# Kernel optimization log

Measured on AMD Instinct MI355X. Metric: run time of the kernel, lower is better.

Reference implementation:

```python
import jax, jax.numpy as jnp
import numpy as np

HIDDEN = 300
DEPTH = 6
ATOM_FDIM = 136
BOND_FDIM = 12
BOND_IN = ATOM_FDIM + BOND_FDIM  # 148
MAX_NB = 6
N_MOLS = 4096
ATOMS_PER_MOL = 32
N_ATOMS = N_MOLS * ATOMS_PER_MOL  # 131072
N_BONDS = 2 * N_ATOMS            # 262144 directed bonds


def setup_inputs() -> dict:
    key = jax.random.key(0)
    ks = jax.random.split(key, 11)
    fatoms = jax.random.normal(ks[0], (N_ATOMS, ATOM_FDIM), jnp.float32)
    fbonds = jax.random.normal(ks[1], (N_BONDS, BOND_IN), jnp.float32)
    agraph = jax.random.randint(ks[2], (N_ATOMS, MAX_NB), 0, N_BONDS, jnp.int32)
    bgraph = jax.random.randint(ks[3], (N_BONDS, MAX_NB), 0, N_BONDS, jnp.int32)
    # Linear weights stored pre-transposed so forward is x @ W
    W_i = jax.random.normal(ks[4], (BOND_IN, HIDDEN), jnp.float32) / np.sqrt(BOND_IN)
    W_h = jax.random.normal(ks[5], (HIDDEN, HIDDEN), jnp.float32) / np.sqrt(HIDDEN)
    W_o = jax.random.normal(ks[6], (ATOM_FDIM + HIDDEN, HIDDEN), jnp.float32) / np.sqrt(ATOM_FDIM + HIDDEN)
    b_o = jax.random.normal(ks[7], (HIDDEN,), jnp.float32) * 0.01
    W_a = jax.random.normal(ks[8], (HIDDEN, HIDDEN), jnp.float32) / np.sqrt(HIDDEN)
    W_b = jax.random.normal(ks[9], (HIDDEN, HIDDEN), jnp.float32) / np.sqrt(HIDDEN)
    b_b = jax.random.normal(ks[10], (HIDDEN,), jnp.float32) * 0.01
    return {"fatoms": fatoms, "fbonds": fbonds, "agraph": agraph, "bgraph": bgraph,
            "W_i": W_i, "W_h": W_h, "W_o": W_o, "b_o": b_o,
            "W_a": W_a, "W_b": W_b, "b_b": b_b}


def reference(fatoms, fbonds, agraph, bgraph, W_i, W_h, W_o, b_o, W_a, W_b, b_b):
    # D-MPNN bond message passing (dropout=0.0 -> identity)
    binput = fbonds @ W_i                         # [N_b, H]
    message = jax.nn.relu(binput)
    for _ in range(DEPTH - 1):
        nei = jnp.take(message, bgraph, axis=0).sum(axis=1)   # gather [N_b, MAX_NB, H] -> sum
        message = jax.nn.relu(binput + nei @ W_h)
    nei_a = jnp.take(message, agraph, axis=0).sum(axis=1)     # [N_a, H]
    atom_hiddens = jax.nn.relu(jnp.concatenate([fatoms, nei_a], axis=1) @ W_o + b_o)
    # Per-molecule self-attention pooling (fixed-size scope: ATOMS_PER_MOL atoms/mol)
    h = atom_hiddens.reshape(N_MOLS, ATOMS_PER_MOL, HIDDEN)   # [B, A, H]
    q = jnp.einsum('bah,hk->bak', h, W_a)
    att = jax.nn.softmax(jnp.einsum('bak,bck->bac', q, h), axis=-1)
    att_h = jax.nn.relu(jnp.einsum('bac,bch->bah', att, h) @ W_b + b_b)
    mol_vecs = (h + att_h).sum(axis=1) / ATOMS_PER_MOL        # [B, H]
    return mol_vecs
```

## Files before the change

### kernel.cpp

```cpp
#include <hip/hip_runtime.h>
#include <hip/hip_fp16.h>
#include <math.h>

#define HIDDEN 300
#define ATOM_FDIM 136
#define BOND_IN 148
#define MAX_NB 6
#define N_MOLS 4096
#define APM 32
#define N_ATOMS (N_MOLS*APM)
#define N_BONDS (2*N_ATOMS)

#define BK 16
#define BM 64
#define ASTR 68
#define BSTR 304

#define WT_C 304
#define WT_K 320

typedef unsigned short u16;
typedef short bf16x8 __attribute__((ext_vector_type(8)));
typedef float f32x4  __attribute__((ext_vector_type(4)));

__device__ float g_scratch[3ull * N_BONDS * HIDDEN + (size_t)N_MOLS * HIDDEN + WT_C * WT_K];

__device__ __forceinline__ u16 bf16_rne(float x) {
    unsigned u = __float_as_uint(x);
    unsigned r = (u + 0x7fffu + ((u >> 16) & 1u)) >> 16;
    return (u16)r;
}
__device__ __forceinline__ float bf16_f(u16 h) {
    return __uint_as_float(((unsigned)h) << 16);
}
__device__ __forceinline__ void st_h4(__half* p, float a, float b, float c, float d) {
    *(__half2*)(p)     = __floats2half2_rn(a, b);
    *(__half2*)(p + 2) = __floats2half2_rn(c, d);
}

__global__ __launch_bounds__(256)
void wt_prep(const float* __restrict__ W, u16* __restrict__ wt_hi, u16* __restrict__ wt_lo)
{
    const int i = blockIdx.x * 256 + threadIdx.x;
    if (i >= WT_C * WT_K) return;
    const int c = i / WT_K, k = i - c * WT_K;
    float w = (c < HIDDEN && k < HIDDEN) ? W[(size_t)k * HIDDEN + c] : 0.f;
    const u16 hi = bf16_rne(w);
    const u16 lo = bf16_rne(w - bf16_f(hi));
    wt_hi[i] = hi;
    wt_lo[i] = lo;
}

__global__ __launch_bounds__(512, 4)
void mp_mfma(const __half* __restrict__ msg,
             const int*   __restrict__ graph,
             const u16*   __restrict__ wt_hi,
             const u16*   __restrict__ wt_lo,
             const __half* __restrict__ binput,
             __half* __restrict__ out0)
{
    __shared__ u16 Ahi[64 * 40];
    __shared__ u16 Alo[64 * 40];
    __shared__ int gx[64 * MAX_NB];

    const int tid  = threadIdx.x;
    const int row0 = blockIdx.x * 64;

    if (tid < 64 * MAX_NB) gx[tid] = graph[(size_t)row0 * MAX_NB + tid];
    __syncthreads();

    const int w  = tid >> 6;
    const int l  = tid & 63;
    const int g  = l >> 4;
    const int mr = (w & 3) * 16 + (l & 15);
    const int tbase = (w >> 2) ? 10 : 0;
    const int ntile = (w >> 2) ? 9 : 10;

    const int sr = tid >> 3;
    const int sk = (tid & 7) * 4;
    const __half* rp0; const __half* rp1; const __half* rp2;
    const __half* rp3; const __half* rp4; const __half* rp5;
    {
        const int* sg = &gx[sr * MAX_NB];
        rp0 = msg + (size_t)sg[0] * HIDDEN + sk;
        rp1 = msg + (size_t)sg[1] * HIDDEN + sk;
        rp2 = msg + (size_t)sg[2] * HIDDEN + sk;
        rp3 = msg + (size_t)sg[3] * HIDDEN + sk;
        rp4 = msg + (size_t)sg[4] * HIDDEN + sk;
        rp5 = msg + (size_t)sg[5] * HIDDEN + sk;
    }

    f32x4 acc[10];
#pragma unroll
    for (int t = 0; t < 10; ++t) acc[t] = (f32x4){0.f, 0.f, 0.f, 0.f};

    uint2 pre[6];
    pre[0] = *(const uint2*)rp0;  pre[1] = *(const uint2*)rp1;
    pre[2] = *(const uint2*)rp2;  pre[3] = *(const uint2*)rp3;
    pre[4] = *(const uint2*)rp4;  pre[5] = *(const uint2*)rp5;

    for (int k0 = 0; k0 < HIDDEN; k0 += 32) {
        float s0 = 0.f, s1 = 0.f, s2 = 0.f, s3 = 0.f;
#pragma unroll
        for (int j = 0; j < 6; ++j) {
            const float2 a0 = __half22float2(*(const __half2*)&pre[j].x);
            const float2 a1 = __half22float2(*(const __half2*)&pre[j].y);
            s0 += a0.x; s1 += a0.y; s2 += a1.x; s3 += a1.y;
        }
        const u16 h0 = bf16_rne(s0), h1 = bf16_rne(s1), h2 = bf16_rne(s2), h3 = bf16_rne(s3);
        const u16 e0 = bf16_rne(s0 - bf16_f(h0)), e1 = bf16_rne(s1 - bf16_f(h1));
        const u16 e2 = bf16_rne(s2 - bf16_f(h2)), e3 = bf16_rne(s3 - bf16_f(h3));
        uint2 ph, pl;
        ph.x = (unsigned)h0 | ((unsigned)h1 << 16);
        ph.y = (unsigned)h2 | ((unsigned)h3 << 16);
        pl.x = (unsigned)e0 | ((unsigned)e1 << 16);
        pl.y = (unsigned)e2 | ((unsigned)e3 << 16);
        *(uint2*)&Ahi[sr * 40 + sk] = ph;
        *(uint2*)&Alo[sr * 40 + sk] = pl;
        __syncthreads();

        const int kn = k0 + 32;
        if (kn < HIDDEN) {
            pre[0] = *(const uint2*)(rp0 + kn);  pre[1] = *(const uint2*)(rp1 + kn);
            pre[2] = *(const uint2*)(rp2 + kn);  pre[3] = *(const uint2*)(rp3 + kn);
            pre[4] = *(const uint2*)(rp4 + kn);  pre[5] = *(const uint2*)(rp5 + kn);
        }

        const bf16x8 ahi = *(const bf16x8*)&Ahi[mr * 40 + 8 * g];
        const bf16x8 alo = *(const bf16x8*)&Alo[mr * 40 + 8 * g];
        const int kb = k0 + 8 * g;
#pragma unroll
        for (int t = 0; t < 10; ++t) {
            if (t < ntile) {
                const int cn = 16 * (tbase + t) + (l & 15);
                const bf16x8 bhi = *(const bf16x8*)&wt_hi[(size_t)cn * WT_K + kb];
                const bf16x8 blo = *(const bf16x8*)&wt_lo[(size_t)cn * WT_K + kb];
                acc[t] = __builtin_amdgcn_mfma_f32_16x16x32_bf16(ahi, bhi, acc[t], 0, 0, 0);
                acc[t] = __builtin_amdgcn_mfma_f32_16x16x32_bf16(ahi, blo, acc[t], 0, 0, 0);
                acc[t] = __builtin_amdgcn_mfma_f32_16x16x32_bf16(alo, bhi, acc[t], 0, 0, 0);
            }
        }
        __syncthreads();
    }

    const u16* bin_u = (const u16*)binput;
#pragma unroll
    for (int t = 0; t < 10; ++t) {
        if (t < ntile) {
            const int col = 16 * (tbase + t) + (l & 15);
            if (col < HIDDEN) {
#pragma unroll
                for (int j = 0; j < 4; ++j) {
                    const size_t off = (size_t)(row0 + (w & 3) * 16 + 4 * g + j) * HIDDEN + col;
                    const u16 raw = __builtin_nontemporal_load(bin_u + off);
                    const float bi = __half2float(__ushort_as_half(raw));
                    out0[off] = __float2half(fmaxf(bi + acc[t][j], 0.f));
                }
            }
        }
    }
}

template<int MODE>
__global__ __launch_bounds__(512)
void gemm_fused(const float* __restrict__ Adense, int lda,
                const void*  __restrict__ msgv,
                const int*   __restrict__ graph,
                const float* __restrict__ W,
                const float* __restrict__ bias,
                const float* __restrict__ hsum,
                float* __restrict__ out0,
                float* __restrict__ out1,
                int K)
{
    __shared__ float As[BK * ASTR];
    __shared__ float Bs[BK * BSTR];
    __shared__ int   gx[BM * MAX_NB];

    const int tid  = threadIdx.x;
    const int wave = tid >> 6;
    const int lane = tid & 63;
    const int row0 = blockIdx.x * BM;
    const int c0   = 4 * lane;
    const bool has4 = (lane < HIDDEN - 256);
    const int  c4   = has4 ? (256 + lane) : 256;

    if (MODE == 2) {
        if (tid < BM * MAX_NB) gx[tid] = graph[(size_t)row0 * MAX_NB + tid];
        __syncthreads();
    }

    float acc[8][5];
#pragma unroll
    for (int r = 0; r < 8; ++r)
#pragma unroll
        for (int c = 0; c < 5; ++c) acc[r][c] = 0.f;

    const int nk = (K + BK - 1) / BK;
    for (int kt = 0; kt < nk; ++kt) {
        const int k0 = kt * BK;
        for (int i = tid; i < BK * 300; i += 512) {
            const int kk = i / 300;
            const int col = i - kk * 300;
            const int k = k0 + kk;
            Bs[kk * BSTR + col] = (k < K) ? W[(size_t)k * HIDDEN + col] : 0.f;
        }
        for (int i = tid; i < BK * BM; i += 512) {
            const int r  = i >> 4;
            const int kk = i & 15;
            const int k  = k0 + kk;
            float v = 0.f;
            if (MODE == 0 || MODE == 3 || MODE == 4) {
                if (k < K) v = Adense[(size_t)(row0 + r) * lda + k];
            } else {
                if (k < ATOM_FDIM) {
                    v = Adense[(size_t)(row0 + r) * lda + k];
                } else if (k < K) {
                    const int kc = k - ATOM_FDIM;
                    const __half* mh = (const __half*)msgv;
#pragma unroll
                    for (int j = 0; j < MAX_NB; ++j)
                        v += __half2float(mh[(size_t)gx[r * MAX_NB + j] * HIDDEN + kc]);
                }
            }
            As[kk * ASTR + r] = v;
        }
        __syncthreads();
#pragma unroll
        for (int kk = 0; kk < BK; ++kk) {
            const float4 bq = *(const float4*)&Bs[kk * BSTR + c0];
            const float  b4 = Bs[kk * BSTR + c4];
            const float4 a0 = *(const float4*)&As[kk * ASTR + wave * 8];
            const float4 a1 = *(const float4*)&As[kk * ASTR + wave * 8 + 4];
            const float ar8[8] = {a0.x, a0.y, a0.z, a0.w, a1.x, a1.y, a1.z, a1.w};
#pragma unroll
            for (int r = 0; r < 8; ++r) {
                acc[r][0] = fmaf(ar8[r], bq.x, acc[r][0]);
                acc[r][1] = fmaf(ar8[r], bq.y, acc[r][1]);
                acc[r][2] = fmaf(ar8[r], bq.z, acc[r][2]);
                acc[r][3] = fmaf(ar8[r], bq.w, acc[r][3]);
                acc[r][4] = fmaf(ar8[r], b4,   acc[r][4]);
            }
        }
        __syncthreads();
    }

    if (MODE == 4) {
        const float4 bqv = *(const float4*)&bias[c0];
        const float  b4v = bias[c4];
        float s0 = 0, s1 = 0, s2 = 0, s3 = 0, s4 = 0;
#pragma unroll
        for (int r = 0; r < 8; ++r) {
            s0 += fmaxf(acc[r][0] + bqv.x, 0.f);
            s1 += fmaxf(acc[r][1] + bqv.y, 0.f);
            s2 += fmaxf(acc[r][2] + bqv.z, 0.f);
            s3 += fmaxf(acc[r][3] + bqv.w, 0.f);
            s4 += fmaxf(acc[r][4] + b4v,   0.f);
        }
        float* wsum = Bs;
        *(float4*)&wsum[wave * BSTR + c0] = make_float4(s0, s1, s2, s3);
        if (has4) wsum[wave * BSTR + c4] = s4;
        __syncthreads();
        const int m0 = blockIdx.x * 2;
        for (int t = tid; t < 2 * HIDDEN; t += 512) {
            const int m = t / HIDDEN, col = t - m * HIDDEN;
            const float v = wsum[(4 * m + 0) * BSTR + col] + wsum[(4 * m + 1) * BSTR + col]
                          + wsum[(4 * m + 2) * BSTR + col] + wsum[(4 * m + 3) * BSTR + col]
                          + hsum[(size_t)(m0 + m) * HIDDEN + col];
            out0[(size_t)(m0 + m) * HIDDEN + col] = v * (1.f / 32.f);
        }
        return;
    }

#pragma unroll
    for (int r = 0; r < 8; ++r) {
        const size_t off = (size_t)(row0 + wave * 8 + r) * HIDDEN;
        float4 v = make_float4(acc[r][0], acc[r][1], acc[r][2], acc[r][3]);
        float v4 = acc[r][4];
        if (MODE == 0) {
            __half* o0 = (__half*)out0;
            __half* o1 = (__half*)out1;
            st_h4(&o0[off + c0], v.x, v.y, v.z, v.w);
            if (has4) o0[off + c4] = __float2half(v4);
            st_h4(&o1[off + c0], fmaxf(v.x,0.f), fmaxf(v.y,0.f), fmaxf(v.z,0.f), fmaxf(v.w,0.f));
            if (has4) o1[off + c4] = __float2half(fmaxf(v4, 0.f));
        } else if (MODE == 2) {
            const float4 bb = *(const float4*)&bias[c0];
            float4 rv = make_float4(fmaxf(v.x+bb.x,0.f), fmaxf(v.y+bb.y,0.f),
                                    fmaxf(v.z+bb.z,0.f), fmaxf(v.w+bb.w,0.f));
            *(float4*)&out0[off + c0] = rv;
            if (has4) out0[off + c4] = fmaxf(v4 + bias[c4], 0.f);
        } else {
            *(float4*)&out0[off + c0] = v;
            if (has4) out0[off + c4] = v4;
        }
    }
}

#define HSTR 320

__device__ __forceinline__ int hsw(int a, int c4u) {
    return a * HSTR + ((c4u ^ (a & 7)) << 2);
}

__global__ __launch_bounds__(512)
void attn_mid(const float* __restrict__ atom_h,
              const float* __restrict__ q_all,
              float* __restrict__ P_all,
              float* __restrict__ hsum)
{
    __shared__ float hs[APM * HSTR];
    __shared__ float qs[APM * HIDDEN];
    __shared__ float att[APM][33];

    const int tid  = threadIdx.x;
    const int wave = tid >> 6;
    const int lane = tid & 63;
    const int mol  = blockIdx.x;
    const float* hb = atom_h + (size_t)mol * APM * HIDDEN;
    const float* qb = q_all  + (size_t)mol * APM * HIDDEN;

    for (int j = tid; j < APM * 75; j += 512) {
        const int a = j / 75, c4u = j - a * 75;
        *(float4*)&hs[hsw(a, c4u)] = *(const float4*)&hb[(size_t)a * HIDDEN + 4 * c4u];
    }
    for (int j = tid; j < APM * 75; j += 512)
        *(float4*)&qs[4 * j] = *(const float4*)&qb[4 * j];
    __syncthreads();

    {
        const int a = tid >> 5, b = tid & 31;
        float s0 = 0.f, s1 = 0.f;
        for (int t = 0; t < 75; ++t) {
            const float4 hv = *(const float4*)&hs[hsw(b, t)];
            const float4 q0 = *(const float4*)&qs[a * HIDDEN + 4 * t];
            const float4 q1 = *(const float4*)&qs[(a + 16) * HIDDEN + 4 * t];
            s0 = fmaf(q0.x, hv.x, fmaf(q0.y, hv.y, fmaf(q0.z, hv.z, fmaf(q0.w, hv.w, s0))));
            s1 = fmaf(q1.x, hv.x, fmaf(q1.y, hv.y, fmaf(q1.z, hv.z, fmaf(q1.w, hv.w, s1))));
        }
        att[a][b] = s0;
        att[a + 16][b] = s1;
    }
    __syncthreads();

    if (tid < APM) {
        float m = -3.4e38f;
#pragma unroll 4
        for (int b = 0; b < APM; ++b) m = fmaxf(m, att[tid][b]);
        float s = 0.f;
#pragma unroll 4
        for (int b = 0; b < APM; ++b) { const float e = __expf(att[tid][b] - m); att[tid][b] = e; s += e; }
        const float inv = 1.f / s;
#pragma unroll 4
        for (int b = 0; b < APM; ++b) att[tid][b] *= inv;
    }
    __syncthreads();

    {
        const int r0 = wave * 4;
        const int c0 = 4 * lane;
        const bool has4 = (lane < 44);
        const int c4u = 64 + (lane >> 2), c4r = lane & 3;
        float4 p[4];
        float  p4[4];
#pragma unroll
        for (int r = 0; r < 4; ++r) { p[r] = make_float4(0,0,0,0); p4[r] = 0.f; }
#pragma unroll 4
        for (int b = 0; b < APM; ++b) {
            const float4 hv = *(const float4*)&hs[hsw(b, lane)];
            const float  h4 = hs[hsw(b, c4u) + c4r];
#pragma unroll
            for (int r = 0; r < 4; ++r) {
                const float av = att[r0 + r][b];
                p[r].x = fmaf(av, hv.x, p[r].x);
                p[r].y = fmaf(av, hv.y, p[r].y);
                p[r].z = fmaf(av, hv.z, p[r].z);
                p[r].w = fmaf(av, hv.w, p[r].w);
                p4[r]  = fmaf(av, h4,   p4[r]);
            }
        }
#pragma unroll
        for (int r = 0; r < 4; ++r) {
            const size_t off = ((size_t)mol * APM + r0 + r) * HIDDEN;
            *(float4*)&P_all[off + c0] = p[r];
            if (has4) P_all[off + 256 + lane] = p4[r];
        }
    }

    if (tid < HIDDEN) {
        const int c4u = tid >> 2, cr = tid & 3;
        float s = 0.f;
#pragma unroll 4
        for (int a = 0; a < APM; ++a) s += hs[hsw(a, c4u) + cr];
        hsum[(size_t)mol * HIDDEN + tid] = s;
    }
}

extern "C" void kernel_launch(void* const* d_in, const int* in_sizes, int n_in,
                              void* d_out, int out_size, void* d_ws, size_t ws_size,
                              hipStream_t stream)
{
    const float* fatoms = (const float*)d_in[0];
    const float* fbonds = (const float*)d_in[1];
    const int*   agraph = (const int*)d_in[2];
    const int*   bgraph = (const int*)d_in[3];
    const float* W_i    = (const float*)d_in[4];
    const float* W_h    = (const float*)d_in[5];
    const float* W_o    = (const float*)d_in[6];
    const float* b_o    = (const float*)d_in[7];
    const float* W_a    = (const float*)d_in[8];
    const float* W_b    = (const float*)d_in[9];
    const float* b_b    = (const float*)d_in[10];
    float* out = (float*)d_out;

    const size_t WB = (size_t)N_BONDS * HIDDEN;
    const size_t WA = (size_t)N_ATOMS * HIDDEN;
    const size_t need = (3 * WB / 2 + 3 * WA + (size_t)N_MOLS * HIDDEN + WT_C * WT_K) * sizeof(float);
    float* base;
    if (ws_size >= need) {
        base = (float*)d_ws;
    } else {
        void* p = nullptr;
        (void)hipGetSymbolAddress(&p, HIP_SYMBOL(g_scratch));
        base = (float*)p;
    }
    __half* binput_h = (__half*)base;
    __half* msgA     = (__half*)(base + WB / 2);
    __half* msgB     = (__half*)(base + WB);
    float*  atom_h   = base + 3 * WB / 2;
    float*  q_all    = atom_h + WA;
    float*  P_all    = q_all + WA;
    float*  hsum     = P_all + WA;
    u16*    wt_hi    = (u16*)(hsum + (size_t)N_MOLS * HIDDEN);
    u16*    wt_lo    = wt_hi + WT_C * WT_K;

    const dim3 blk(512);

    wt_prep<<<(WT_C * WT_K + 255) / 256, dim3(256), 0, stream>>>(W_h, wt_hi, wt_lo);

    gemm_fused<0><<<N_BONDS / BM, blk, 0, stream>>>(
        fbonds, BOND_IN, nullptr, nullptr, W_i, nullptr, nullptr,
        (float*)binput_h, (float*)msgA, BOND_IN);

    const __half* cur = msgA;
    __half* nxt = msgB;
    for (int it = 0; it < 5; ++it) {
        mp_mfma<<<N_BONDS / 64, blk, 0, stream>>>(
            cur, bgraph, wt_hi, wt_lo, binput_h, nxt);
        __half* t = nxt; nxt = (__half*)cur; cur = t;
    }

    gemm_fused<2><<<N_ATOMS / BM, blk, 0, stream>>>(
        fatoms, ATOM_FDIM, (const void*)cur, agraph, W_o, b_o, nullptr,
        atom_h, nullptr, ATOM_FDIM + HIDDEN);

    gemm_fused<3><<<N_ATOMS / BM, blk, 0, stream>>>(
        atom_h, HIDDEN, nullptr, nullptr, W_a, nullptr, nullptr,
        q_all, nullptr, HIDDEN);

    attn_mid<<<N_MOLS, dim3(512), 0, stream>>>(atom_h, q_all, P_all, hsum);

    gemm_fused<4><<<N_ATOMS / BM, blk, 0, stream>>>(
        P_all, HIDDEN, nullptr, nullptr, W_b, b_b, hsum,
        out, nullptr, HIDDEN);
}
```

Baseline: 7.188 ms.

## Split message-passing GEMM into two K-half passes with fp16 partial buffer

```diff
diff --git a/kernel.cpp b/kernel.cpp
--- a/kernel.cpp
+++ b/kernel.cpp
@@ -23,7 +23,8 @@
 typedef short bf16x8 __attribute__((ext_vector_type(8)));
 typedef float f32x4  __attribute__((ext_vector_type(4)));
 
-__device__ float g_scratch[3ull * N_BONDS * HIDDEN + (size_t)N_MOLS * HIDDEN + WT_C * WT_K];
+__device__ float g_scratch[2ull * N_BONDS * HIDDEN + 3ull * N_ATOMS * HIDDEN
+                           + (size_t)N_MOLS * HIDDEN + WT_C * WT_K];
 
 __device__ __forceinline__ u16 bf16_rne(float x) {
     unsigned u = __float_as_uint(x);
@@ -51,13 +52,16 @@
     wt_lo[i] = lo;
 }
 
+template<int PASS>
 __global__ __launch_bounds__(512, 4)
 void mp_mfma(const __half* __restrict__ msg,
              const int*   __restrict__ graph,
              const u16*   __restrict__ wt_hi,
              const u16*   __restrict__ wt_lo,
              const __half* __restrict__ binput,
-             __half* __restrict__ out0)
+             __half* __restrict__ accb,
+             __half* __restrict__ out0,
+             int kbeg)
 {
     __shared__ u16 Ahi[64 * 40];
     __shared__ u16 Alo[64 * 40];
@@ -94,18 +98,24 @@
 #pragma unroll
     for (int t = 0; t < 10; ++t) acc[t] = (f32x4){0.f, 0.f, 0.f, 0.f};
 
-    uint2 pre[6];
-    pre[0] = *(const uint2*)rp0;  pre[1] = *(const uint2*)rp1;
-    pre[2] = *(const uint2*)rp2;  pre[3] = *(const uint2*)rp3;
-    pre[4] = *(const uint2*)rp4;  pre[5] = *(const uint2*)rp5;
-
-    for (int k0 = 0; k0 < HIDDEN; k0 += 32) {
+#pragma unroll
+    for (int s = 0; s < 5; ++s) {
+        const int k0 = kbeg + 32 * s;
         float s0 = 0.f, s1 = 0.f, s2 = 0.f, s3 = 0.f;
-#pragma unroll
-        for (int j = 0; j < 6; ++j) {
-            const float2 a0 = __half22float2(*(const __half2*)&pre[j].x);
-            const float2 a1 = __half22float2(*(const __half2*)&pre[j].y);
-            s0 += a0.x; s1 += a0.y; s2 += a1.x; s3 += a1.y;
+        {
+            const uint2 q0 = *(const uint2*)(rp0 + k0);
+            const uint2 q1 = *(const uint2*)(rp1 + k0);
+            const uint2 q2 = *(const uint2*)(rp2 + k0);
+            const uint2 q3 = *(const uint2*)(rp3 + k0);
+            const uint2 q4 = *(const uint2*)(rp4 + k0);
+            const uint2 q5 = *(const uint2*)(rp5 + k0);
+            const uint2 qs[6] = {q0, q1, q2, q3, q4, q5};
+#pragma unroll
+            for (int j = 0; j < 6; ++j) {
+                const float2 a0 = __half22float2(*(const __half2*)&qs[j].x);
+                const float2 a1 = __half22float2(*(const __half2*)&qs[j].y);
+                s0 += a0.x; s1 += a0.y; s2 += a1.x; s3 += a1.y;
+            }
         }
         const u16 h0 = bf16_rne(s0), h1 = bf16_rne(s1), h2 = bf16_rne(s2), h3 = bf16_rne(s3);
         const u16 e0 = bf16_rne(s0 - bf16_f(h0)), e1 = bf16_rne(s1 - bf16_f(h1));
@@ -119,13 +129,6 @@
         *(uint2*)&Alo[sr * 40 + sk] = pl;
         __syncthreads();
 
-        const int kn = k0 + 32;
-        if (kn < HIDDEN) {
-            pre[0] = *(const uint2*)(rp0 + kn);  pre[1] = *(const uint2*)(rp1 + kn);
-            pre[2] = *(const uint2*)(rp2 + kn);  pre[3] = *(const uint2*)(rp3 + kn);
-            pre[4] = *(const uint2*)(rp4 + kn);  pre[5] = *(const uint2*)(rp5 + kn);
-        }
-
         const bf16x8 ahi = *(const bf16x8*)&Ahi[mr * 40 + 8 * g];
         const bf16x8 alo = *(const bf16x8*)&Alo[mr * 40 + 8 * g];
         const int kb = k0 + 8 * g;
@@ -144,6 +147,7 @@
     }
 
     const u16* bin_u = (const u16*)binput;
+    const u16* acc_u = (const u16*)accb;
 #pragma unroll
     for (int t = 0; t < 10; ++t) {
         if (t < ntile) {
@@ -152,9 +156,16 @@
 #pragma unroll
                 for (int j = 0; j < 4; ++j) {
                     const size_t off = (size_t)(row0 + (w & 3) * 16 + 4 * g + j) * HIDDEN + col;
-                    const u16 raw = __builtin_nontemporal_load(bin_u + off);
-                    const float bi = __half2float(__ushort_as_half(raw));
-                    out0[off] = __float2half(fmaxf(bi + acc[t][j], 0.f));
+                    if (PASS == 0) {
+                        const __half hv = __float2half(acc[t][j]);
+                        __builtin_nontemporal_store(__half_as_ushort(hv), (u16*)&accb[off]);
+                    } else {
+                        const float bi = __half2float(__ushort_as_half(
+                            __builtin_nontemporal_load(bin_u + off)));
+                        const float ac = __half2float(__ushort_as_half(
+                            __builtin_nontemporal_load(acc_u + off)));
+                        out0[off] = __float2half(fmaxf(bi + ac + acc[t][j], 0.f));
+                    }
                 }
             }
         }
@@ -415,7 +426,7 @@
 
     const size_t WB = (size_t)N_BONDS * HIDDEN;
     const size_t WA = (size_t)N_ATOMS * HIDDEN;
-    const size_t need = (3 * WB / 2 + 3 * WA + (size_t)N_MOLS * HIDDEN + WT_C * WT_K) * sizeof(float);
+    const size_t need = (2 * WB + 3 * WA + (size_t)N_MOLS * HIDDEN + WT_C * WT_K) * sizeof(float);
     float* base;
     if (ws_size >= need) {
         base = (float*)d_ws;
@@ -427,7 +438,8 @@
     __half* binput_h = (__half*)base;
     __half* msgA     = (__half*)(base + WB / 2);
     __half* msgB     = (__half*)(base + WB);
-    float*  atom_h   = base + 3 * WB / 2;
+    __half* acc_h    = (__half*)(base + 3 * WB / 2);
+    float*  atom_h   = base + 2 * WB;
     float*  q_all    = atom_h + WA;
     float*  P_all    = q_all + WA;
     float*  hsum     = P_all + WA;
@@ -445,8 +457,10 @@
     const __half* cur = msgA;
     __half* nxt = msgB;
     for (int it = 0; it < 5; ++it) {
-        mp_mfma<<<N_BONDS / 64, blk, 0, stream>>>(
-            cur, bgraph, wt_hi, wt_lo, binput_h, nxt);
+        mp_mfma<0><<<N_BONDS / 64, blk, 0, stream>>>(
+            cur, bgraph, wt_hi, wt_lo, binput_h, acc_h, nullptr, 0);
+        mp_mfma<1><<<N_BONDS / 64, blk, 0, stream>>>(
+            cur, bgraph, wt_hi, wt_lo, binput_h, acc_h, nxt, 160);
         __half* t = nxt; nxt = (__half*)cur; cur = t;
     }
 
```

After: 7.877 ms. 1.1x slower.
